# Performance work log

Hardware: AMD Instinct MI355X
Metric: run time of the kernel (lower is better)

Reference implementation:

```python
import jax, jax.numpy as jnp
import numpy as np

CH = 8       # MASK_HEAD.HEAD_CHANNELS
IN_CH = 8    # MASK_BRANCH.OUT_CHANNELS
MASK_OUT_STRIDE = 4
SOI = jnp.array([64.0, 128.0, 256.0, 512.0, 1024.0], dtype=jnp.float32)


def _upsample_ac(x, factor, axis):
    # align_corners=True bilinear upsample along one axis: L -> factor*(L-1)+1
    L = x.shape[axis]
    M = factor * (L - 1) + 1
    pos = jnp.arange(M, dtype=jnp.float32) / factor
    i0 = jnp.floor(pos).astype(jnp.int32)
    i1 = jnp.minimum(i0 + 1, L - 1)
    frac = pos - i0.astype(jnp.float32)
    x0 = jnp.take(x, i0, axis=axis)
    x1 = jnp.take(x, i1, axis=axis)
    sh = [1] * x.ndim
    sh[axis] = M
    frac = frac.reshape(sh)
    return x0 * (1.0 - frac) + x1 * frac


def aligned_bilinear(x, factor):
    # x: [n, 1, H, W] -> [n, 1, factor*H, factor*W] (AdelaiDet aligned_bilinear)
    if factor == 1:
        return x
    h, w = x.shape[2], x.shape[3]
    x = jnp.pad(x, ((0, 0), (0, 0), (0, 1), (0, 1)), mode='edge')
    x = _upsample_ac(x, factor, 2)
    x = _upsample_ac(x, factor, 3)
    p = factor // 2
    x = jnp.pad(x, ((0, 0), (0, 0), (p, 0), (p, 0)), mode='edge')
    return x[:, :, :factor * h, :factor * w]


def setup_inputs() -> dict:
    key = jax.random.key(0)
    k1, k2, k3, k4, k5, k6 = jax.random.split(key, 6)
    N, H, W = 4, 128, 128
    n_inst = 400
    num_gen = (IN_CH + 2) * CH + CH + CH * CH + CH + CH * 1 + 1  # 169
    return {
        'mask_feats': jax.random.normal(k1, (N, IN_CH, H, W), dtype=jnp.float32),
        'mask_shift': jax.random.uniform(k2, (H * W, 2), dtype=jnp.float32),
        'shifts': jax.random.uniform(k3, (n_inst, 2), dtype=jnp.float32),
        'inst_params': jax.random.normal(k4, (n_inst, num_gen), dtype=jnp.float32),
        'im_inds': jax.random.randint(k5, (n_inst,), 0, N, dtype=jnp.int32),
        'fpn_levels': jax.random.randint(k6, (n_inst,), 0, 5, dtype=jnp.int32),
        'mask_feat_stride': 8,
    }


def reference(mask_feats, mask_shift, shifts, inst_params, im_inds, fpn_levels, mask_feat_stride):
    n = inst_params.shape[0]
    N, C, H, W = mask_feats.shape
    # relative coords: [n, 2, H*W]
    rel = shifts[:, None, :] - mask_shift[None, :, :]          # [n, HW, 2]
    rel = jnp.transpose(rel, (0, 2, 1))                        # [n, 2, HW]
    rel = rel / SOI[fpn_levels][:, None, None]
    feats = mask_feats[im_inds].reshape(n, C, H * W)           # [n, C, HW]
    x = jnp.concatenate([rel, feats], axis=1)                  # [n, C+2, HW]
    # parse dynamic params: weights first, then biases
    w1 = inst_params[:, 0:80].reshape(n, CH, IN_CH + 2)
    w2 = inst_params[:, 80:144].reshape(n, CH, CH)
    w3 = inst_params[:, 144:152].reshape(n, 1, CH)
    b1 = inst_params[:, 152:160]
    b2 = inst_params[:, 160:168]
    b3 = inst_params[:, 168:169]
    # per-instance 1x1 convs == batched tiny GEMMs
    x = jax.nn.relu(jnp.einsum('noc,ncp->nop', w1, x) + b1[:, :, None])
    x = jax.nn.relu(jnp.einsum('noc,ncp->nop', w2, x) + b2[:, :, None])
    x = jnp.einsum('noc,ncp->nop', w3, x) + b3[:, :, None]
    logits = x.reshape(n, 1, H, W)
    factor = int(mask_feat_stride) // MASK_OUT_STRIDE
    return aligned_bilinear(logits, factor)
```

## Files before the change

kernel.cpp:

```cpp
#include <hip/hip_runtime.h>


#define HW 16384
#define NP 169

__global__ __launch_bounds__(256)
void pack_kernel(const float* __restrict__ mf, float* __restrict__ rec)
{
    const int g   = blockIdx.x * 256 + threadIdx.x;
    const int img = g >> 14;
    const int p   = g & 16383;
    const float* fb = mf + (size_t)img * 8 * HW + p;
    float4 a = make_float4(fb[0],      fb[HW],     fb[2 * HW], fb[3 * HW]);
    float4 b = make_float4(fb[4 * HW], fb[5 * HW], fb[6 * HW], fb[7 * HW]);
    float4* o = (float4*)(rec + (size_t)g * 8);
    o[0] = a;
    o[1] = b;
}

__global__ __launch_bounds__(256, 6)
void dmh_kernel(const float* __restrict__ mask_feats,
                const float* __restrict__ mask_shift,
                const float* __restrict__ shifts,
                const float* __restrict__ inst_params,
                const int*   __restrict__ im_inds,
                const int*   __restrict__ fpn_levels,
                const float* __restrict__ rec,
                float*       __restrict__ out,
                int use_rec)
{
    __shared__ float lgE[17 * 64];
    __shared__ float lgO[17 * 64];

    const int bx   = blockIdx.x;
    const int inst = bx >> 3;
    const int rg   = bx & 7;
    const int tid  = threadIdx.x;
    const int r0   = rg * 16;

    const int img = im_inds[inst];
    const float* __restrict__ wp = inst_params + (size_t)inst * NP;
    const float s0  = shifts[2 * inst];
    const float s1  = shifts[2 * inst + 1];
    const float inv = 1.0f / (float)(64 << fpn_levels[inst]);
    const float* __restrict__ fb = mask_feats + (size_t)img * 8 * HW;
    const float* __restrict__ rb = rec + (size_t)img * 8 * HW;

    auto load_px = [&](int p, float* x) {
        const int t = p >> 7;
        const int c = p & 127;
        const int r = min(max(r0 - 1 + t, 0), 127);
        const int g = r * 128 + c;
        const float2 ms = *(const float2*)(mask_shift + 2 * g);
        x[0] = (s0 - ms.x) * inv;
        x[1] = (s1 - ms.y) * inv;
        if (use_rec) {
            const float4* q = (const float4*)(rb + (size_t)g * 8);
            const float4 a = q[0], b = q[1];
            x[2] = a.x; x[3] = a.y; x[4] = a.z; x[5] = a.w;
            x[6] = b.x; x[7] = b.y; x[8] = b.z; x[9] = b.w;
        } else {
            #pragma unroll
            for (int k = 0; k < 8; ++k) x[2 + k] = fb[k * HW + g];
        }
    };

    auto store_px = [&](int p, float v) {
        const int t = p >> 7;
        const int c = p & 127;
        const int idx = t * 64 + (c >> 1);
        if (c & 1) lgO[idx] = v; else lgE[idx] = v;
    };

    #pragma unroll
    for (int u = 0; u < 4; ++u) {
        const int pA = tid + 512 * u;
        const int pB = pA + 256;
        float xa[10], xb[10];
        load_px(pA, xa);
        load_px(pB, xb);

        float ya[8], yb[8];
        #pragma unroll
        for (int o = 0; o < 8; ++o) {
            const float bia = wp[152 + o];
            float a = bia, b = bia;
            #pragma unroll
            for (int c = 0; c < 10; ++c) {
                const float w = wp[o * 10 + c];
                a = fmaf(w, xa[c], a);
                b = fmaf(w, xb[c], b);
            }
            ya[o] = fmaxf(a, 0.f);
            yb[o] = fmaxf(b, 0.f);
        }
        float za[8], zb[8];
        #pragma unroll
        for (int o = 0; o < 8; ++o) {
            const float bia = wp[160 + o];
            float a = bia, b = bia;
            #pragma unroll
            for (int c = 0; c < 8; ++c) {
                const float w = wp[80 + o * 8 + c];
                a = fmaf(w, ya[c], a);
                b = fmaf(w, yb[c], b);
            }
            za[o] = fmaxf(a, 0.f);
            zb[o] = fmaxf(b, 0.f);
        }
        float va = wp[168], vb = va;
        #pragma unroll
        for (int c = 0; c < 8; ++c) {
            const float w = wp[144 + c];
            va = fmaf(w, za[c], va);
            vb = fmaf(w, zb[c], vb);
        }
        store_px(pA, va);
        store_px(pB, vb);
    }

    if (tid < 128) {
        const int p = 2048 + tid;
        float x[10];
        load_px(p, x);
        float y1[8];
        #pragma unroll
        for (int o = 0; o < 8; ++o) {
            float a = wp[152 + o];
            #pragma unroll
            for (int c = 0; c < 10; ++c) a = fmaf(wp[o * 10 + c], x[c], a);
            y1[o] = fmaxf(a, 0.f);
        }
        float y2[8];
        #pragma unroll
        for (int o = 0; o < 8; ++o) {
            float a = wp[160 + o];
            #pragma unroll
            for (int c = 0; c < 8; ++c) a = fmaf(wp[80 + o * 8 + c], y1[c], a);
            y2[o] = fmaxf(a, 0.f);
        }
        float v = wp[168];
        #pragma unroll
        for (int c = 0; c < 8; ++c) v = fmaf(wp[144 + c], y2[c], v);
        store_px(p, v);
    }

    __syncthreads();

    float* __restrict__ op =
        out + (size_t)inst * 65536 + (size_t)(2 * r0) * 256;
    const int w = tid >> 6;
    const int l = tid & 63;
    const int parity = w & 1;

    #pragma unroll
    for (int j = 0; j < 8; ++j) {
        const int p2 = (w >> 1) + 2 * j;
        const int yl = 2 * p2 + parity;
        float4 res;
        if (parity) {
            const float* e = lgE + (p2 + 1) * 64;
            const float* o = lgO + (p2 + 1) * 64;
            const float v0 = e[l];
            const float v1 = o[l];
            const float vm = (l > 0) ? o[l - 1] : v0;
            res = make_float4(0.5f * (vm + v0), v0, 0.5f * (v0 + v1), v1);
        } else {
            const float* eA = lgE + p2 * 64;
            const float* oA = lgO + p2 * 64;
            const float* eB = eA + 64;
            const float* oB = oA + 64;
            const float v0A = eA[l], v1A = oA[l];
            const float v0B = eB[l], v1B = oB[l];
            const float vmA = (l > 0) ? oA[l - 1] : v0A;
            const float vmB = (l > 0) ? oB[l - 1] : v0B;
            res = make_float4(0.25f * (vmA + v0A + vmB + v0B),
                              0.5f  * (v0A + v0B),
                              0.25f * (v0A + v1A + v0B + v1B),
                              0.5f  * (v1A + v1B));
        }
        *(float4*)(op + yl * 256 + 4 * l) = res;
    }
}

extern "C" void kernel_launch(void* const* d_in, const int* in_sizes, int n_in,
                              void* d_out, int out_size, void* d_ws, size_t ws_size,
                              hipStream_t stream) {
    (void)n_in; (void)out_size;
    const float* mask_feats  = (const float*)d_in[0];
    const float* mask_shift  = (const float*)d_in[1];
    const float* shifts      = (const float*)d_in[2];
    const float* inst_params = (const float*)d_in[3];
    const int*   im_inds     = (const int*)d_in[4];
    const int*   fpn_levels  = (const int*)d_in[5];
    float* out = (float*)d_out;
    float* rec = (float*)d_ws;

    const int n_inst = in_sizes[2] / 2;
    const size_t rec_bytes = (size_t)4 * HW * 8 * sizeof(float);
    const int use_rec = (ws_size >= rec_bytes) ? 1 : 0;

    if (use_rec)
        pack_kernel<<<dim3(4 * HW / 256), dim3(256), 0, stream>>>(
            mask_feats, rec);

    dmh_kernel<<<dim3(n_inst * 8), dim3(256), 0, stream>>>(
        mask_feats, mask_shift, shifts, inst_params, im_inds, fpn_levels,
        rec, out, use_rec);
}
```

Measured before the change: 152.6 us.

## Pack mask_shift into per-pixel record and use nontemporal output stores

```diff
diff --git a/kernel.cpp b/kernel.cpp
--- a/kernel.cpp
+++ b/kernel.cpp
@@ -3,31 +3,32 @@
 
 #define HW 16384
 #define NP 169
+#define RECW 12
+
+typedef float nf4 __attribute__((ext_vector_type(4)));
 
 __global__ __launch_bounds__(256)
-void pack_kernel(const float* __restrict__ mf, float* __restrict__ rec)
+void pack_kernel(const float* __restrict__ mf, const float* __restrict__ msf,
+                 float* __restrict__ rec)
 {
     const int g   = blockIdx.x * 256 + threadIdx.x;
     const int img = g >> 14;
     const int p   = g & 16383;
     const float* fb = mf + (size_t)img * 8 * HW + p;
-    float4 a = make_float4(fb[0],      fb[HW],     fb[2 * HW], fb[3 * HW]);
-    float4 b = make_float4(fb[4 * HW], fb[5 * HW], fb[6 * HW], fb[7 * HW]);
-    float4* o = (float4*)(rec + (size_t)g * 8);
-    o[0] = a;
-    o[1] = b;
+    const float2 ms = *(const float2*)(msf + 2 * p);
+    float4* o = (float4*)(rec + (size_t)g * RECW);
+    o[0] = make_float4(ms.x, ms.y, fb[0], fb[HW]);
+    o[1] = make_float4(fb[2 * HW], fb[3 * HW], fb[4 * HW], fb[5 * HW]);
+    o[2] = make_float4(fb[6 * HW], fb[7 * HW], 0.f, 0.f);
 }
 
 __global__ __launch_bounds__(256, 6)
-void dmh_kernel(const float* __restrict__ mask_feats,
-                const float* __restrict__ mask_shift,
-                const float* __restrict__ shifts,
+void dmh_kernel(const float* __restrict__ shifts,
                 const float* __restrict__ inst_params,
                 const int*   __restrict__ im_inds,
                 const int*   __restrict__ fpn_levels,
                 const float* __restrict__ rec,
-                float*       __restrict__ out,
-                int use_rec)
+                float*       __restrict__ out)
 {
     __shared__ float lgE[17 * 64];
     __shared__ float lgO[17 * 64];
@@ -38,31 +39,24 @@
     const int tid  = threadIdx.x;
     const int r0   = rg * 16;
 
-    const int img = im_inds[inst];
     const float* __restrict__ wp = inst_params + (size_t)inst * NP;
     const float s0  = shifts[2 * inst];
     const float s1  = shifts[2 * inst + 1];
     const float inv = 1.0f / (float)(64 << fpn_levels[inst]);
-    const float* __restrict__ fb = mask_feats + (size_t)img * 8 * HW;
-    const float* __restrict__ rb = rec + (size_t)img * 8 * HW;
+    const float* __restrict__ rb = rec + (size_t)im_inds[inst] * HW * RECW;
 
     auto load_px = [&](int p, float* x) {
         const int t = p >> 7;
         const int c = p & 127;
         const int r = min(max(r0 - 1 + t, 0), 127);
         const int g = r * 128 + c;
-        const float2 ms = *(const float2*)(mask_shift + 2 * g);
-        x[0] = (s0 - ms.x) * inv;
-        x[1] = (s1 - ms.y) * inv;
-        if (use_rec) {
-            const float4* q = (const float4*)(rb + (size_t)g * 8);
-            const float4 a = q[0], b = q[1];
-            x[2] = a.x; x[3] = a.y; x[4] = a.z; x[5] = a.w;
-            x[6] = b.x; x[7] = b.y; x[8] = b.z; x[9] = b.w;
-        } else {
-            #pragma unroll
-            for (int k = 0; k < 8; ++k) x[2 + k] = fb[k * HW + g];
-        }
+        const float4* q = (const float4*)(rb + (size_t)g * RECW);
+        const float4 a = q[0], b = q[1], d = q[2];
+        x[0] = (s0 - a.x) * inv;
+        x[1] = (s1 - a.y) * inv;
+        x[2] = a.z; x[3] = a.w;
+        x[4] = b.x; x[5] = b.y; x[6] = b.z; x[7] = b.w;
+        x[8] = d.x; x[9] = d.y;
     };
 
     auto store_px = [&](int p, float v) {
@@ -157,14 +151,14 @@
     for (int j = 0; j < 8; ++j) {
         const int p2 = (w >> 1) + 2 * j;
         const int yl = 2 * p2 + parity;
-        float4 res;
+        nf4 res;
         if (parity) {
             const float* e = lgE + (p2 + 1) * 64;
             const float* o = lgO + (p2 + 1) * 64;
             const float v0 = e[l];
             const float v1 = o[l];
             const float vm = (l > 0) ? o[l - 1] : v0;
-            res = make_float4(0.5f * (vm + v0), v0, 0.5f * (v0 + v1), v1);
+            res = (nf4){0.5f * (vm + v0), v0, 0.5f * (v0 + v1), v1};
         } else {
             const float* eA = lgE + p2 * 64;
             const float* oA = lgO + p2 * 64;
@@ -174,19 +168,19 @@
             const float v0B = eB[l], v1B = oB[l];
             const float vmA = (l > 0) ? oA[l - 1] : v0A;
             const float vmB = (l > 0) ? oB[l - 1] : v0B;
-            res = make_float4(0.25f * (vmA + v0A + vmB + v0B),
-                              0.5f  * (v0A + v0B),
-                              0.25f * (v0A + v1A + v0B + v1B),
-                              0.5f  * (v1A + v1B));
-        }
-        *(float4*)(op + yl * 256 + 4 * l) = res;
+            res = (nf4){0.25f * (vmA + v0A + vmB + v0B),
+                        0.5f  * (v0A + v0B),
+                        0.25f * (v0A + v1A + v0B + v1B),
+                        0.5f  * (v1A + v1B)};
+        }
+        __builtin_nontemporal_store(res, (nf4*)(op + yl * 256 + 4 * l));
     }
 }
 
 extern "C" void kernel_launch(void* const* d_in, const int* in_sizes, int n_in,
                               void* d_out, int out_size, void* d_ws, size_t ws_size,
                               hipStream_t stream) {
-    (void)n_in; (void)out_size;
+    (void)n_in; (void)out_size; (void)ws_size;
     const float* mask_feats  = (const float*)d_in[0];
     const float* mask_shift  = (const float*)d_in[1];
     const float* shifts      = (const float*)d_in[2];
@@ -197,14 +191,10 @@
     float* rec = (float*)d_ws;
 
     const int n_inst = in_sizes[2] / 2;
-    const size_t rec_bytes = (size_t)4 * HW * 8 * sizeof(float);
-    const int use_rec = (ws_size >= rec_bytes) ? 1 : 0;
-
-    if (use_rec)
-        pack_kernel<<<dim3(4 * HW / 256), dim3(256), 0, stream>>>(
-            mask_feats, rec);
+
+    pack_kernel<<<dim3(4 * HW / 256), dim3(256), 0, stream>>>(
+        mask_feats, mask_shift, rec);
 
     dmh_kernel<<<dim3(n_inst * 8), dim3(256), 0, stream>>>(
-        mask_feats, mask_shift, shifts, inst_params, im_inds, fpn_levels,
-        rec, out, use_rec);
+        shifts, inst_params, im_inds, fpn_levels, rec, out);
 }
```

Measured after the change: 173.7 us. 13.8% more time.
